# Kernel tuning notes

Hardware: AMD Instinct MI355X
Metric: run time of the kernel (lower is better)

The kernel has to match this reference:

```python
import jax, jax.numpy as jnp
import numpy as np


def setup_inputs() -> dict:
    key = jax.random.key(0)
    k1, k2, k3 = jax.random.split(key, 3)
    B, S, D_IN, D_OUT = 4, 2048, 4096, 4096
    x = jax.random.normal(k1, (B, S, D_IN), dtype=jnp.float32)
    weight = jax.random.normal(k2, (D_OUT, D_IN), dtype=jnp.float32)
    bias = jax.random.normal(k3, (D_OUT,), dtype=jnp.float32)
    return {"x": x, "weight": weight, "bias": bias}


def reference(x, weight, bias):
    # 1-bit quantize weights to {-1, 0, +1} via sign (STE is backward-only).
    qw = jnp.sign(weight)  # [out, in]
    # F.linear: x @ qw.T + bias
    out = jnp.einsum('bsd,od->bso', x, qw) + bias
    return out
```

## Files before the change

kernel.cpp:

```cpp
#include <hip/hip_runtime.h>
#include <hip/hip_bf16.h>
#include <stdint.h>

typedef unsigned short u16;
typedef unsigned int u32;
typedef __attribute__((ext_vector_type(8))) short short8;
typedef __attribute__((ext_vector_type(4))) float f32x4;
typedef __attribute__((ext_vector_type(4))) int i32x4;

static __device__ __forceinline__ u16 f2bf(float f) {
  union { __hip_bfloat16 b; u16 u; } c;
  c.b = __float2bfloat16(f);
  return c.u;
}
static __device__ __forceinline__ float bf2f(u16 u) {
  return __uint_as_float(((u32)u) << 16);
}

__global__ __launch_bounds__(256) void prep_x_i8(const float* __restrict__ X,
                                                 char* __restrict__ A1,
                                                 char* __restrict__ A2) {
  const u32 t = blockIdx.x * 256 + threadIdx.x;
  const float4 v = ((const float4*)X)[t];
  const float vv[4] = {v.x, v.y, v.z, v.w};
  u32 p1 = 0, p2 = 0;
#pragma unroll
  for (int j = 0; j < 4; ++j) {
    float q1f = rintf(vv[j] * 16.f);
    q1f = fminf(fmaxf(q1f, -127.f), 127.f);
    const float r = vv[j] - q1f * 0.0625f;
    float q2f = rintf(r * 4096.f);
    q2f = fminf(fmaxf(q2f, -127.f), 127.f);
    p1 |= ((u32)((int)q1f & 0xFF)) << (8 * j);
    p2 |= ((u32)((int)q2f & 0xFF)) << (8 * j);
  }
  ((u32*)A1)[t] = p1;
  ((u32*)A2)[t] = p2;
}

__global__ __launch_bounds__(256) void prep_w_i8(const float* __restrict__ W,
                                                 char* __restrict__ Qw) {
  const u32 t = blockIdx.x * 256 + threadIdx.x;
  const float4 v = ((const float4*)W)[t];
  const float vv[4] = {v.x, v.y, v.z, v.w};
  u32 p = 0;
#pragma unroll
  for (int j = 0; j < 4; ++j) {
    const u32 b = __float_as_uint(vv[j]);
    const int q = ((b << 1) == 0) ? 0 : ((b >> 31) ? -1 : 1);
    p |= ((u32)(q & 0xFF)) << (8 * j);
  }
  ((u32*)Qw)[t] = p;
}

#define LGKM0 asm volatile("s_waitcnt lgkmcnt(0)" ::: "memory")
#define VMCNT(n) asm volatile("s_waitcnt vmcnt(" #n ")" ::: "memory")
#define CFENCE asm volatile("" ::: "memory")
#define BAR do { __builtin_amdgcn_s_barrier(); CFENCE; } while (0)

static __device__ __forceinline__ void gload16(const void* g, void* l) {
  __builtin_amdgcn_global_load_lds(
      (const __attribute__((address_space(1))) u32*)g,
      (__attribute__((address_space(3))) u32*)l, 16, 0, 0);
}

template <int PASS>
__global__ __launch_bounds__(512, 2)
void gemm256_i8(const char* __restrict__ A, const char* __restrict__ B,
                const float* __restrict__ Bias, float* __restrict__ C) {
  __shared__ __align__(16) unsigned char ldsc[131072];

  const int tid = threadIdx.x;
  const int lane = tid & 63;
  const int wid = tid >> 6;
  const int wm = wid >> 2;
  const int wn = wid & 3;
  const int r16 = lane & 15;
  const int khalf = lane >> 4;

  const int bid = blockIdx.x;
  const int swz = (bid & 7) * 64 + (bid >> 3);
  const int brow = swz >> 4;
  const int bcol = swz & 15;

  const u32 Lcol = (u32)(((tid & 7) ^ ((tid >> 3) & 7)) * 16);
  const char* Ag = (const char*)A;
  const char* Bg = (const char*)B;
  const u32 a_g0 = (u32)(brow * 256 + (tid >> 3)) * 4096u + Lcol;
  const u32 b_g0 = (u32)(bcol * 256 + (tid >> 3)) * 4096u + Lcol;
  char* const lc = (char*)ldsc;
  const u32 l_t = (u32)tid * 16u;

  const u32 col0 = (u32)(((khalf << 4) ^ ((r16 & 7) << 4)));
  const u32 arow0 = (u32)(wm * 64 + r16) * 128u;
  const u32 brow0 = (u32)(wn * 64 + r16) * 128u + 65536u;

  i32x4 acc[8][4];
#pragma unroll
  for (int m = 0; m < 8; ++m)
#pragma unroll
    for (int n = 0; n < 4; ++n)
#pragma unroll
      for (int j = 0; j < 4; ++j) acc[m][n][j] = 0;
  i32x4 bq[4][2];

#define AOFF(P, MF, KK) ((u32)((P)*32768) + arow0 + \
    (u32)((((MF) >> 2) * 16384) + (((MF) & 3) * 2048)) + (col0 ^ ((KK) << 6)))
#define BOFF(P, NF, KK) (brow0 + (u32)((P)*32768) + (u32)((NF)*2048) + (col0 ^ ((KK) << 6)))
#define RD(off) (*(const i32x4*)(lc + (off)))

#define STAGE_A(TP, H, PB) do { \
    const char* g_ = Ag + a_g0 + (u32)((H)*128*4096) + (u32)(TP)*128u; \
    char* l_ = lc + (u32)((PB)*32768 + (H)*16384) + l_t; \
    gload16(g_, l_); gload16(g_ + 64*4096, l_ + 8192); } while (0)

#define STAGE_B(TP, H, PB) do { \
    const char* g_ = Bg + b_g0 + (u32)((H)*128*4096) + (u32)(TP)*128u; \
    char* l_ = lc + 65536u + (u32)((PB)*32768 + (H)*16384) + l_t; \
    gload16(g_, l_); gload16(g_ + 64*4096, l_ + 8192); } while (0)

#define MM4(MF, A0, A1r) do { \
    _Pragma("unroll") for (int nf_ = 0; nf_ < 4; ++nf_) { \
      acc[MF][nf_] = __builtin_amdgcn_mfma_i32_16x16x64_i8(A0, bq[nf_][0], acc[MF][nf_], 0, 0, 0); \
      acc[MF][nf_] = __builtin_amdgcn_mfma_i32_16x16x64_i8(A1r, bq[nf_][1], acc[MF][nf_], 0, 0, 0); } } while (0)

#define PHASE0(P, S) do { \
    S; \
    const i32x4 a00 = RD(AOFF(P, 0, 0)), a01 = RD(AOFF(P, 0, 1)); \
    const i32x4 a10 = RD(AOFF(P, 1, 0)), a11 = RD(AOFF(P, 1, 1)); \
    _Pragma("unroll") for (int nf_ = 0; nf_ < 4; ++nf_) { \
      bq[nf_][0] = RD(BOFF(P, nf_, 0)); bq[nf_][1] = RD(BOFF(P, nf_, 1)); } \
    BAR; LGKM0; __builtin_amdgcn_sched_barrier(0); \
    __builtin_amdgcn_s_setprio(1); MM4(0, a00, a01); MM4(1, a10, a11); \
    __builtin_amdgcn_s_setprio(0); BAR; } while (0)

#define PHASEX(P, MF0, S, TW) do { \
    S; \
    const i32x4 a00 = RD(AOFF(P, MF0, 0)), a01 = RD(AOFF(P, MF0, 1)); \
    const i32x4 a10 = RD(AOFF(P, (MF0)+1, 0)), a11 = RD(AOFF(P, (MF0)+1, 1)); \
    BAR; LGKM0; __builtin_amdgcn_sched_barrier(0); \
    __builtin_amdgcn_s_setprio(1); MM4(MF0, a00, a01); MM4((MF0)+1, a10, a11); \
    __builtin_amdgcn_s_setprio(0); TW; BAR; } while (0)

  STAGE_A(0, 0, 0); STAGE_A(0, 1, 0); STAGE_B(0, 0, 0); STAGE_B(0, 1, 0);
  STAGE_A(1, 0, 1); STAGE_B(1, 0, 1); STAGE_B(1, 1, 1);
  VMCNT(6); BAR;

  int T = 0;
#pragma unroll 1
  for (int it = 0; it < 15; ++it) {
    PHASE0(0, STAGE_A(T + 1, 1, 1));
    PHASEX(0, 2, STAGE_B(T + 2, 0, 0), );
    PHASEX(0, 4, STAGE_B(T + 2, 1, 0), );
    PHASEX(0, 6, STAGE_A(T + 2, 0, 0), VMCNT(6));
    PHASE0(1, STAGE_A(T + 2, 1, 0));
    PHASEX(1, 2, STAGE_B(T + 3, 0, 1), );
    PHASEX(1, 4, STAGE_B(T + 3, 1, 1), );
    PHASEX(1, 6, STAGE_A(T + 3, 0, 1), VMCNT(6));
    T += 2;
  }
  PHASE0(0, STAGE_A(31, 1, 1));
  PHASEX(0, 2, , );
  PHASEX(0, 4, , );
  PHASEX(0, 6, , VMCNT(0));
  PHASE0(1, );
  PHASEX(1, 2, , );
  PHASEX(1, 4, , );
  PHASEX(1, 6, , );

  const int ccol0 = bcol * 256 + wn * 64 + r16;
  float bb[4];
#pragma unroll
  for (int nf = 0; nf < 4; ++nf) bb[nf] = Bias[ccol0 + nf * 16];
  const int crow_base = brow * 256 + wm * 64 + khalf * 4;
  const float scale = (PASS == 0) ? 0.0625f : (1.0f / 4096.0f);
#pragma unroll
  for (int mf = 0; mf < 8; ++mf) {
    const int row = crow_base + (mf >> 2) * 128 + (mf & 3) * 16;
#pragma unroll
    for (int nf = 0; nf < 4; ++nf) {
      const int col = ccol0 + nf * 16;
#pragma unroll
      for (int j = 0; j < 4; ++j) {
        const size_t idx = (size_t)(row + j) * 4096 + col;
        if (PASS == 0) {
          C[idx] = (float)acc[mf][nf][j] * scale;
        } else {
          C[idx] = C[idx] + (float)acc[mf][nf][j] * scale + bb[nf];
        }
      }
    }
  }
#undef AOFF
#undef BOFF
#undef RD
#undef STAGE_A
#undef STAGE_B
#undef MM4
#undef PHASE0
#undef PHASEX
}

#define BM 128
#define BN 128
#define BK 32
#define LDKP 40

__global__ __launch_bounds__(256, 2)
void bitnet_gemm_fallback(const float* __restrict__ X, const float* __restrict__ W,
                          const float* __restrict__ Bias, float* __restrict__ C,
                          int M, int N, int K) {
  __shared__ u16 AsH[BM][LDKP];
  __shared__ u16 AsL[BM][LDKP];
  __shared__ u16 Bs[BN][LDKP];
  const int nwg = gridDim.x;
  const int bid = blockIdx.x;
  const int swz = ((nwg & 7) == 0) ? ((bid & 7) * (nwg >> 3) + (bid >> 3)) : bid;
  const int nbn = N / BN;
  const int brow = swz / nbn;
  const int bcol = swz % nbn;
  const int tid = threadIdx.x;
  const int lane = tid & 63;
  const int wid = tid >> 6;
  const int wr = wid >> 1;
  const int wc = wid & 1;
  const int srow = tid >> 2;
  const int skc = (tid & 3) * 8;
  const float* Ab = X + (size_t)brow * BM * K;
  const float* Bb = W + (size_t)bcol * BN * K;
  f32x4 acc[4][4];
#pragma unroll
  for (int m = 0; m < 4; ++m)
#pragma unroll
    for (int n = 0; n < 4; ++n)
#pragma unroll
      for (int j = 0; j < 4; ++j) acc[m][n][j] = 0.f;
  const int r0 = lane & 15;
  const int k0 = (lane >> 4) * 8;
  for (int kt = 0; kt < K; kt += BK) {
    __syncthreads();
#pragma unroll
    for (int p = 0; p < 2; ++p) {
      const int row = p * 64 + srow;
      const float* src = Ab + (size_t)row * K + kt + skc;
      const float4 v0 = *(const float4*)(src);
      const float4 v1 = *(const float4*)(src + 4);
      const float v[8] = {v0.x, v0.y, v0.z, v0.w, v1.x, v1.y, v1.z, v1.w};
      short8 ph, pl;
#pragma unroll
      for (int j = 0; j < 8; ++j) {
        const u16 h = f2bf(v[j]);
        const float rem = v[j] - bf2f(h);
        ph[j] = (short)h;
        pl[j] = (short)f2bf(rem);
      }
      *(short8*)&AsH[row][skc] = ph;
      *(short8*)&AsL[row][skc] = pl;
    }
#pragma unroll
    for (int p = 0; p < 2; ++p) {
      const int row = p * 64 + srow;
      const float* src = Bb + (size_t)row * K + kt + skc;
      const float4 v0 = *(const float4*)(src);
      const float4 v1 = *(const float4*)(src + 4);
      const float v[8] = {v0.x, v0.y, v0.z, v0.w, v1.x, v1.y, v1.z, v1.w};
      short8 pq;
#pragma unroll
      for (int j = 0; j < 8; ++j) {
        const u32 b = __float_as_uint(v[j]);
        const u16 q = ((b << 1) == 0) ? (u16)0 : (u16)(0x3F80u | ((b >> 16) & 0x8000u));
        pq[j] = (short)q;
      }
      *(short8*)&Bs[row][skc] = pq;
    }
    __syncthreads();
    short8 ah[4], al[4], bqf[4];
#pragma unroll
    for (int m = 0; m < 4; ++m) {
      ah[m] = *(const short8*)&AsH[wr * 64 + m * 16 + r0][k0];
      al[m] = *(const short8*)&AsL[wr * 64 + m * 16 + r0][k0];
    }
#pragma unroll
    for (int n = 0; n < 4; ++n)
      bqf[n] = *(const short8*)&Bs[wc * 64 + n * 16 + r0][k0];
#pragma unroll
    for (int m = 0; m < 4; ++m)
#pragma unroll
      for (int n = 0; n < 4; ++n) {
        acc[m][n] = __builtin_amdgcn_mfma_f32_16x16x32_bf16(ah[m], bqf[n], acc[m][n], 0, 0, 0);
        acc[m][n] = __builtin_amdgcn_mfma_f32_16x16x32_bf16(al[m], bqf[n], acc[m][n], 0, 0, 0);
      }
  }
  const int rbase = (lane >> 4) * 4;
  const int crow0 = brow * BM + wr * 64;
  const int ccol0 = bcol * BN + wc * 64;
#pragma unroll
  for (int n = 0; n < 4; ++n) {
    const int col = ccol0 + n * 16 + r0;
    const float bbv = Bias[col];
#pragma unroll
    for (int m = 0; m < 4; ++m) {
      const int row = crow0 + m * 16 + rbase;
#pragma unroll
      for (int j = 0; j < 4; ++j) {
        C[(size_t)(row + j) * N + col] = acc[m][n][j] + bbv;
      }
    }
  }
}

extern "C" void kernel_launch(void* const* d_in, const int* in_sizes, int n_in,
                              void* d_out, int out_size, void* d_ws, size_t ws_size,
                              hipStream_t stream) {
  const float* X = (const float*)d_in[0];
  const float* W = (const float*)d_in[1];
  const float* Bias = (const float*)d_in[2];
  float* C = (float*)d_out;

  const int N = in_sizes[2];
  const int K = in_sizes[1] / N;
  const int M = in_sizes[0] / K;

  const size_t a_bytes = (size_t)M * K;
  const size_t qw_bytes = (size_t)N * K;

  if (M == 8192 && N == 4096 && K == 4096 && ws_size >= 2 * a_bytes + qw_bytes) {
    char* A1 = (char*)d_ws;
    char* A2 = A1 + a_bytes;
    char* Qw = A2 + a_bytes;
    prep_x_i8<<<(M * K) / (4 * 256), 256, 0, stream>>>(X, A1, A2);
    prep_w_i8<<<(N * K) / (4 * 256), 256, 0, stream>>>(W, Qw);
    const int grid = (M / 256) * (N / 256);
    gemm256_i8<0><<<grid, 512, 0, stream>>>(A1, Qw, Bias, C);
    gemm256_i8<1><<<grid, 512, 0, stream>>>(A2, Qw, Bias, C);
  } else {
    bitnet_gemm_fallback<<<(M / BM) * (N / BN), 256, 0, stream>>>(X, W, Bias, C, M, N, K);
  }
}
```

Before: 518.7 us.

## Fuse two int8 GEMM passes into one kernel sharing weight tiles

The two per-residual int8 GEMM launches are replaced by a single kernel that loads both activation terms (A1, A2) alongside one weight tile and keeps two accumulator sets. The output tile is now 256x128, and the epilogue combines both scaled terms with the bias in one write. This removes the second read of the weights and the read-modify-write of C. The two prep kernels are also merged into one launch. In exchange, the K step is halved to 64, which doubles the barrier count, and the B tile per block is smaller.

Measured after the change: 566.9 us. 9.3% more time.

```diff
diff --git a/kernel.cpp b/kernel.cpp
--- a/kernel.cpp
+++ b/kernel.cpp
@@ -17,40 +17,42 @@
   return __uint_as_float(((u32)u) << 16);
 }
 
-__global__ __launch_bounds__(256) void prep_x_i8(const float* __restrict__ X,
-                                                 char* __restrict__ A1,
-                                                 char* __restrict__ A2) {
+__global__ __launch_bounds__(256) void prep_all(const float* __restrict__ X,
+                                                const float* __restrict__ W,
+                                                char* __restrict__ A1,
+                                                char* __restrict__ A2,
+                                                char* __restrict__ Qw) {
   const u32 t = blockIdx.x * 256 + threadIdx.x;
-  const float4 v = ((const float4*)X)[t];
-  const float vv[4] = {v.x, v.y, v.z, v.w};
-  u32 p1 = 0, p2 = 0;
-#pragma unroll
-  for (int j = 0; j < 4; ++j) {
-    float q1f = rintf(vv[j] * 16.f);
-    q1f = fminf(fmaxf(q1f, -127.f), 127.f);
-    const float r = vv[j] - q1f * 0.0625f;
-    float q2f = rintf(r * 4096.f);
-    q2f = fminf(fmaxf(q2f, -127.f), 127.f);
-    p1 |= ((u32)((int)q1f & 0xFF)) << (8 * j);
-    p2 |= ((u32)((int)q2f & 0xFF)) << (8 * j);
-  }
-  ((u32*)A1)[t] = p1;
-  ((u32*)A2)[t] = p2;
-}
-
-__global__ __launch_bounds__(256) void prep_w_i8(const float* __restrict__ W,
-                                                 char* __restrict__ Qw) {
-  const u32 t = blockIdx.x * 256 + threadIdx.x;
-  const float4 v = ((const float4*)W)[t];
-  const float vv[4] = {v.x, v.y, v.z, v.w};
-  u32 p = 0;
-#pragma unroll
-  for (int j = 0; j < 4; ++j) {
-    const u32 b = __float_as_uint(vv[j]);
-    const int q = ((b << 1) == 0) ? 0 : ((b >> 31) ? -1 : 1);
-    p |= ((u32)(q & 0xFF)) << (8 * j);
-  }
-  ((u32*)Qw)[t] = p;
+  const u32 NX = 8388608u;
+  if (t < NX) {
+    const float4 v = ((const float4*)X)[t];
+    const float vv[4] = {v.x, v.y, v.z, v.w};
+    u32 p1 = 0, p2 = 0;
+#pragma unroll
+    for (int j = 0; j < 4; ++j) {
+      float q1f = rintf(vv[j] * 16.f);
+      q1f = fminf(fmaxf(q1f, -127.f), 127.f);
+      const float r = vv[j] - q1f * 0.0625f;
+      float q2f = rintf(r * 4096.f);
+      q2f = fminf(fmaxf(q2f, -127.f), 127.f);
+      p1 |= ((u32)((int)q1f & 0xFF)) << (8 * j);
+      p2 |= ((u32)((int)q2f & 0xFF)) << (8 * j);
+    }
+    ((u32*)A1)[t] = p1;
+    ((u32*)A2)[t] = p2;
+  } else {
+    const u32 tw = t - NX;
+    const float4 v = ((const float4*)W)[tw];
+    const float vv[4] = {v.x, v.y, v.z, v.w};
+    u32 p = 0;
+#pragma unroll
+    for (int j = 0; j < 4; ++j) {
+      const u32 b = __float_as_uint(vv[j]);
+      const int q = ((b << 1) == 0) ? 0 : ((b >> 31) ? -1 : 1);
+      p |= ((u32)(q & 0xFF)) << (8 * j);
+    }
+    ((u32*)Qw)[tw] = p;
+  }
 }
 
 #define LGKM0 asm volatile("s_waitcnt lgkmcnt(0)" ::: "memory")
@@ -64,146 +66,133 @@
       (__attribute__((address_space(3))) u32*)l, 16, 0, 0);
 }
 
-template <int PASS>
 __global__ __launch_bounds__(512, 2)
-void gemm256_i8(const char* __restrict__ A, const char* __restrict__ B,
-                const float* __restrict__ Bias, float* __restrict__ C) {
-  __shared__ __align__(16) unsigned char ldsc[131072];
+void gemm_fused_i8(const char* __restrict__ A1, const char* __restrict__ A2,
+                   const char* __restrict__ B, const float* __restrict__ Bias,
+                   float* __restrict__ C) {
+  __shared__ __align__(16) unsigned char ldsc[81920];
+  char* const lc = (char*)ldsc;
 
   const int tid = threadIdx.x;
   const int lane = tid & 63;
   const int wid = tid >> 6;
-  const int wm = wid >> 2;
-  const int wn = wid & 3;
+  const int wm = wid >> 1;
+  const int wn = wid & 1;
   const int r16 = lane & 15;
-  const int khalf = lane >> 4;
+  const int kq = lane >> 4;
 
   const int bid = blockIdx.x;
-  const int swz = (bid & 7) * 64 + (bid >> 3);
-  const int brow = swz >> 4;
-  const int bcol = swz & 15;
-
-  const u32 Lcol = (u32)(((tid & 7) ^ ((tid >> 3) & 7)) * 16);
-  const char* Ag = (const char*)A;
-  const char* Bg = (const char*)B;
-  const u32 a_g0 = (u32)(brow * 256 + (tid >> 3)) * 4096u + Lcol;
-  const u32 b_g0 = (u32)(bcol * 256 + (tid >> 3)) * 4096u + Lcol;
-  char* const lc = (char*)ldsc;
+  const int swz = (bid & 7) * 128 + (bid >> 3);
+  const int brow = swz >> 5;
+  const int bcol = swz & 31;
+
+  const int srp = tid >> 3;
+  const int sc = (tid & 7) ^ (srp & 7);
+  const u32 srcoff = (u32)(srp * 2 + (sc >> 2)) * 4096u + (u32)((sc & 3) * 16);
+  const char* Ag1 = A1 + (size_t)(brow * 256) * 4096 + srcoff;
+  const char* Ag2 = A2 + (size_t)(brow * 256) * 4096 + srcoff;
+  const char* Bgp = B + (size_t)(bcol * 128) * 4096 + srcoff;
   const u32 l_t = (u32)tid * 16u;
 
-  const u32 col0 = (u32)(((khalf << 4) ^ ((r16 & 7) << 4)));
-  const u32 arow0 = (u32)(wm * 64 + r16) * 128u;
-  const u32 brow0 = (u32)(wn * 64 + r16) * 128u + 65536u;
-
-  i32x4 acc[8][4];
-#pragma unroll
-  for (int m = 0; m < 8; ++m)
+  const u32 slot = (u32)(((((r16 & 1) * 4) + kq) ^ (r16 >> 1)) * 16);
+  const u32 aBase = (u32)(wm * 4096 + (r16 >> 1) * 128) + slot;
+  const u32 bBase = 32768u + (u32)(wn * 4096 + (r16 >> 1) * 128) + slot;
+
+  i32x4 acc1[4][4], acc2[4][4];
+#pragma unroll
+  for (int m = 0; m < 4; ++m)
 #pragma unroll
     for (int n = 0; n < 4; ++n)
 #pragma unroll
-      for (int j = 0; j < 4; ++j) acc[m][n][j] = 0;
-  i32x4 bq[4][2];
-
-#define AOFF(P, MF, KK) ((u32)((P)*32768) + arow0 + \
-    (u32)((((MF) >> 2) * 16384) + (((MF) & 3) * 2048)) + (col0 ^ ((KK) << 6)))
-#define BOFF(P, NF, KK) (brow0 + (u32)((P)*32768) + (u32)((NF)*2048) + (col0 ^ ((KK) << 6)))
+      for (int j = 0; j < 4; ++j) { acc1[m][n][j] = 0; acc2[m][n][j] = 0; }
+  i32x4 bq[4];
+
 #define RD(off) (*(const i32x4*)(lc + (off)))
-
-#define STAGE_A(TP, H, PB) do { \
-    const char* g_ = Ag + a_g0 + (u32)((H)*128*4096) + (u32)(TP)*128u; \
-    char* l_ = lc + (u32)((PB)*32768 + (H)*16384) + l_t; \
-    gload16(g_, l_); gload16(g_ + 64*4096, l_ + 8192); } while (0)
-
-#define STAGE_B(TP, H, PB) do { \
-    const char* g_ = Bg + b_g0 + (u32)((H)*128*4096) + (u32)(TP)*128u; \
-    char* l_ = lc + 65536u + (u32)((PB)*32768 + (H)*16384) + l_t; \
-    gload16(g_, l_); gload16(g_ + 64*4096, l_ + 8192); } while (0)
-
-#define MM4(MF, A0, A1r) do { \
+#define ARD(P, TERM, MF) RD((u32)((P)*40960 + (TERM)*16384 + (MF)*1024) + aBase)
+#define BRD(P, NF) RD((u32)((P)*40960 + (NF)*1024) + bBase)
+
+#define ST_A1(T, H, P) gload16(Ag1 + (size_t)(H)*128*4096 + (u32)(T)*64, \
+                               lc + (u32)((P)*40960 + (H)*8192) + l_t)
+#define ST_A2(T, H, P) gload16(Ag2 + (size_t)(H)*128*4096 + (u32)(T)*64, \
+                               lc + (u32)((P)*40960 + 16384 + (H)*8192) + l_t)
+#define ST_B(T, P) gload16(Bgp + (u32)(T)*64, lc + (u32)((P)*40960 + 32768) + l_t)
+
+#define MFMA16(ACC, A0v, A1v, A2v, A3v) do { \
     _Pragma("unroll") for (int nf_ = 0; nf_ < 4; ++nf_) { \
-      acc[MF][nf_] = __builtin_amdgcn_mfma_i32_16x16x64_i8(A0, bq[nf_][0], acc[MF][nf_], 0, 0, 0); \
-      acc[MF][nf_] = __builtin_amdgcn_mfma_i32_16x16x64_i8(A1r, bq[nf_][1], acc[MF][nf_], 0, 0, 0); } } while (0)
-
-#define PHASE0(P, S) do { \
+      ACC[0][nf_] = __builtin_amdgcn_mfma_i32_16x16x64_i8(A0v, bq[nf_], ACC[0][nf_], 0, 0, 0); \
+      ACC[1][nf_] = __builtin_amdgcn_mfma_i32_16x16x64_i8(A1v, bq[nf_], ACC[1][nf_], 0, 0, 0); \
+      ACC[2][nf_] = __builtin_amdgcn_mfma_i32_16x16x64_i8(A2v, bq[nf_], ACC[2][nf_], 0, 0, 0); \
+      ACC[3][nf_] = __builtin_amdgcn_mfma_i32_16x16x64_i8(A3v, bq[nf_], ACC[3][nf_], 0, 0, 0); \
+    } } while (0)
+
+#define PH0(P, S) do { \
     S; \
-    const i32x4 a00 = RD(AOFF(P, 0, 0)), a01 = RD(AOFF(P, 0, 1)); \
-    const i32x4 a10 = RD(AOFF(P, 1, 0)), a11 = RD(AOFF(P, 1, 1)); \
-    _Pragma("unroll") for (int nf_ = 0; nf_ < 4; ++nf_) { \
-      bq[nf_][0] = RD(BOFF(P, nf_, 0)); bq[nf_][1] = RD(BOFF(P, nf_, 1)); } \
+    const i32x4 a0 = ARD(P, 0, 0), a1v = ARD(P, 0, 1); \
+    const i32x4 a2v = ARD(P, 0, 2), a3v = ARD(P, 0, 3); \
+    bq[0] = BRD(P, 0); bq[1] = BRD(P, 1); bq[2] = BRD(P, 2); bq[3] = BRD(P, 3); \
     BAR; LGKM0; __builtin_amdgcn_sched_barrier(0); \
-    __builtin_amdgcn_s_setprio(1); MM4(0, a00, a01); MM4(1, a10, a11); \
+    __builtin_amdgcn_s_setprio(1); MFMA16(acc1, a0, a1v, a2v, a3v); \
     __builtin_amdgcn_s_setprio(0); BAR; } while (0)
 
-#define PHASEX(P, MF0, S, TW) do { \
+#define PH1(P, S, TW) do { \
     S; \
-    const i32x4 a00 = RD(AOFF(P, MF0, 0)), a01 = RD(AOFF(P, MF0, 1)); \
-    const i32x4 a10 = RD(AOFF(P, (MF0)+1, 0)), a11 = RD(AOFF(P, (MF0)+1, 1)); \
+    const i32x4 a0 = ARD(P, 1, 0), a1v = ARD(P, 1, 1); \
+    const i32x4 a2v = ARD(P, 1, 2), a3v = ARD(P, 1, 3); \
     BAR; LGKM0; __builtin_amdgcn_sched_barrier(0); \
-    __builtin_amdgcn_s_setprio(1); MM4(MF0, a00, a01); MM4((MF0)+1, a10, a11); \
+    __builtin_amdgcn_s_setprio(1); MFMA16(acc2, a0, a1v, a2v, a3v); \
     __builtin_amdgcn_s_setprio(0); TW; BAR; } while (0)
 
-  STAGE_A(0, 0, 0); STAGE_A(0, 1, 0); STAGE_B(0, 0, 0); STAGE_B(0, 1, 0);
-  STAGE_A(1, 0, 1); STAGE_B(1, 0, 1); STAGE_B(1, 1, 1);
-  VMCNT(6); BAR;
+  ST_A1(0, 0, 0); ST_A1(0, 1, 0); ST_A2(0, 0, 0); ST_A2(0, 1, 0); ST_B(0, 0);
+  ST_A1(1, 0, 1); ST_A1(1, 1, 1); ST_B(1, 1);
+  VMCNT(3); BAR;
 
   int T = 0;
 #pragma unroll 1
-  for (int it = 0; it < 15; ++it) {
-    PHASE0(0, STAGE_A(T + 1, 1, 1));
-    PHASEX(0, 2, STAGE_B(T + 2, 0, 0), );
-    PHASEX(0, 4, STAGE_B(T + 2, 1, 0), );
-    PHASEX(0, 6, STAGE_A(T + 2, 0, 0), VMCNT(6));
-    PHASE0(1, STAGE_A(T + 2, 1, 0));
-    PHASEX(1, 2, STAGE_B(T + 3, 0, 1), );
-    PHASEX(1, 4, STAGE_B(T + 3, 1, 1), );
-    PHASEX(1, 6, STAGE_A(T + 3, 0, 1), VMCNT(6));
+  for (int it = 0; it < 31; ++it) {
+    PH0(0, { ST_A2(T + 1, 0, 1); ST_A2(T + 1, 1, 1); });
+    PH1(0, { ST_B(T + 2, 0); ST_A1(T + 2, 0, 0); ST_A1(T + 2, 1, 0); }, VMCNT(3));
+    PH0(1, { ST_A2(T + 2, 0, 0); ST_A2(T + 2, 1, 0); });
+    PH1(1, { ST_B(T + 3, 1); ST_A1(T + 3, 0, 1); ST_A1(T + 3, 1, 1); }, VMCNT(3));
     T += 2;
   }
-  PHASE0(0, STAGE_A(31, 1, 1));
-  PHASEX(0, 2, , );
-  PHASEX(0, 4, , );
-  PHASEX(0, 6, , VMCNT(0));
-  PHASE0(1, );
-  PHASEX(1, 2, , );
-  PHASEX(1, 4, , );
-  PHASEX(1, 6, , );
-
-  const int ccol0 = bcol * 256 + wn * 64 + r16;
+  PH0(0, { ST_A2(63, 0, 1); ST_A2(63, 1, 1); });
+  PH1(0, , VMCNT(0));
+  PH0(1, );
+  PH1(1, , );
+
+  const int ccol0 = bcol * 128 + wn * 64 + r16;
   float bb[4];
 #pragma unroll
   for (int nf = 0; nf < 4; ++nf) bb[nf] = Bias[ccol0 + nf * 16];
-  const int crow_base = brow * 256 + wm * 64 + khalf * 4;
-  const float scale = (PASS == 0) ? 0.0625f : (1.0f / 4096.0f);
-#pragma unroll
-  for (int mf = 0; mf < 8; ++mf) {
-    const int row = crow_base + (mf >> 2) * 128 + (mf & 3) * 16;
+  const int crow0 = brow * 256 + wm * 64 + kq * 4;
+#pragma unroll
+  for (int mf = 0; mf < 4; ++mf) {
+    const int row = crow0 + mf * 16;
 #pragma unroll
     for (int nf = 0; nf < 4; ++nf) {
       const int col = ccol0 + nf * 16;
 #pragma unroll
       for (int j = 0; j < 4; ++j) {
-        const size_t idx = (size_t)(row + j) * 4096 + col;
-        if (PASS == 0) {
-          C[idx] = (float)acc[mf][nf][j] * scale;
-        } else {
-          C[idx] = C[idx] + (float)acc[mf][nf][j] * scale + bb[nf];
-        }
-      }
-    }
-  }
-#undef AOFF
-#undef BOFF
+        C[(size_t)(row + j) * 4096 + col] =
+            (float)acc1[mf][nf][j] * 0.0625f +
+            (float)acc2[mf][nf][j] * (1.0f / 4096.0f) + bb[nf];
+      }
+    }
+  }
 #undef RD
-#undef STAGE_A
-#undef STAGE_B
-#undef MM4
-#undef PHASE0
-#undef PHASEX
+#undef ARD
+#undef BRD
+#undef ST_A1
+#undef ST_A2
+#undef ST_B
+#undef MFMA16
+#undef PH0
+#undef PH1
 }
 
 #define BM 128
 #define BN 128
-#define BK 32
+#define BKF 32
 #define LDKP 40
 
 __global__ __launch_bounds__(256, 2)
@@ -237,7 +226,7 @@
       for (int j = 0; j < 4; ++j) acc[m][n][j] = 0.f;
   const int r0 = lane & 15;
   const int k0 = (lane >> 4) * 8;
-  for (int kt = 0; kt < K; kt += BK) {
+  for (int kt = 0; kt < K; kt += BKF) {
     __syncthreads();
 #pragma unroll
     for (int p = 0; p < 2; ++p) {
@@ -328,11 +317,10 @@
     char* A1 = (char*)d_ws;
     char* A2 = A1 + a_bytes;
     char* Qw = A2 + a_bytes;
-    prep_x_i8<<<(M * K) / (4 * 256), 256, 0, stream>>>(X, A1, A2);
-    prep_w_i8<<<(N * K) / (4 * 256), 256, 0, stream>>>(W, Qw);
-    const int grid = (M / 256) * (N / 256);
-    gemm256_i8<0><<<grid, 512, 0, stream>>>(A1, Qw, Bias, C);
-    gemm256_i8<1><<<grid, 512, 0, stream>>>(A2, Qw, Bias, C);
+    const int prep_grid = (int)((a_bytes + qw_bytes) / 4 / 256);
+    prep_all<<<prep_grid, 256, 0, stream>>>(X, W, A1, A2, Qw);
+    const int grid = (M / 256) * (N / 128);
+    gemm_fused_i8<<<grid, 512, 0, stream>>>(A1, A2, Qw, Bias, C);
   } else {
     bitnet_gemm_fallback<<<(M / BM) * (N / BN), 256, 0, stream>>>(X, W, Bias, C, M, N, K);
   }
```
